# Performance work log

Measured on AMD Instinct MI355X. Metric: run time of the kernel, lower is better.

The kernel has to match this reference:

```python
import jax, jax.numpy as jnp
import numpy as np

# Static problem sizes
B, C, T, H, W = 2, 256, 16, 64, 64
N = 128                      # number of ROIs
OT, OH, OW = 2, 7, 7         # output_size (t, h, w)
SS, TS = 1.0, 1.0            # spatial_scale, temporal_scale
T_EXT_MAX, S_EXT_MAX = 16, 32  # max ROI extents (by construction of rois)
# adaptive_max_pool bin length is bounded by ceil(L/O)+1
KT = (T_EXT_MAX + OT - 1) // OT + 1   # 9
KS = (S_EXT_MAX + OH - 1) // OH + 1   # 6


def setup_inputs() -> dict:
    key = jax.random.key(0)
    features = jax.random.normal(key, (B, C, T, H, W), dtype=jnp.float32)
    rng = np.random.default_rng(0)
    bidx = rng.integers(0, B, N)
    te = rng.integers(4, T_EXT_MAX + 1, N)
    t1 = rng.integers(0, T - te + 1)
    t2 = t1 + te - 1
    he = rng.integers(8, S_EXT_MAX + 1, N)
    y1 = rng.integers(0, H - he + 1)
    y2 = y1 + he - 1
    we = rng.integers(8, S_EXT_MAX + 1, N)
    x1 = rng.integers(0, W - we + 1)
    x2 = x1 + we - 1
    # layout: (batch_idx, t1, x1, y1, t2, x2, y2)
    rois = np.stack([bidx, t1, x1, y1, t2, x2, y2], axis=1).astype(np.float32)
    return {"features": features, "rois": jnp.asarray(rois)}


def _bin_idx(start, length, O, K):
    """Adaptive-pool bin indices for one dim. Returns abs indices [O,K] and validity mask."""
    o = jnp.arange(O)
    s = (o * length) // O                      # floor(o*L/O)
    e = ((o + 1) * length + O - 1) // O        # ceil((o+1)*L/O)
    idx = s[:, None] + jnp.arange(K)[None, :]  # [O, K]
    valid = idx < e[:, None]
    return start + jnp.minimum(idx, length - 1), valid


def _pool_one(roi, features):
    b = roi[0].astype(jnp.int32)
    # source scales coords cols [1,2,3,4] by spatial_scale and [0,5] by temporal_scale
    scale = jnp.array([TS, SS, SS, SS, SS, TS], dtype=roi.dtype)
    c = jnp.floor(roi[1:7] * scale).astype(jnp.int32)
    t1, x1, y1, t2, x2, y2 = c[0], c[1], c[2], c[3], c[4], c[5]
    feat = features[b]  # [C, T, H, W]
    neg = -jnp.inf
    # W dimension
    wi, wv = _bin_idx(x1, x2 - x1 + 1, OW, KS)
    x = feat[:, :, :, wi]                                    # [C,T,H,OW,KS]
    x = jnp.where(wv, x, neg).max(axis=-1)                   # [C,T,H,OW]
    # H dimension
    hi, hv = _bin_idx(y1, y2 - y1 + 1, OH, KS)
    x = jnp.take(x, hi.reshape(-1), axis=2).reshape(C, T, OH, KS, OW)
    x = jnp.where(hv[None, None, :, :, None], x, neg).max(axis=3)  # [C,T,OH,OW]
    # T dimension
    ti, tv = _bin_idx(t1, t2 - t1 + 1, OT, KT)
    x = jnp.take(x, ti.reshape(-1), axis=1).reshape(C, OT, KT, OH, OW)
    return jnp.where(tv[None, :, :, None, None], x, neg).max(axis=2)  # [C,OT,OH,OW]


def reference(features, rois):
    # sequential map over ROIs keeps peak memory bounded (each ROI pool is fully vectorized)
    return jax.lax.map(lambda r: _pool_one(r, features), rois)  # [N,C,OT,OH,OW]
```

## Files before the change

### kernel.cpp

```cpp
#include <hip/hip_runtime.h>
#include <hip/hip_fp16.h>
#include <math.h>

#define BB 2
#define CC 256
#define TT 16
#define HH 64
#define WW 64
#define NN 128
#define OT 2
#define OH 7
#define OW 7
#define PP (TT * HH * WW)
#define BIN (OT * OH * OW)
#define CU2 (CC / 2)
#define GRIDP (NN * OH * OW / 4)

typedef _Float16 hf2 __attribute__((ext_vector_type(2)));

__global__ __launch_bounds__(256) void transpose_f16_kernel(
    const float* __restrict__ in, unsigned int* __restrict__ outt )
{
    __shared__ float tile[64][65];
    int pb = blockIdx.x & 1023;
    int cb = (blockIdx.x >> 10) & 3;
    int b  = blockIdx.x >> 12;

    int tx = threadIdx.x & 63;
    int wv = threadIdx.x >> 6;
    const float* src = in + ((size_t)b * CC + cb * 64) * PP + pb * 64;
    #pragma unroll
    for (int r = 0; r < 16; ++r) {
        int c = wv + r * 4;
        tile[tx][c] = src[(size_t)c * PP + tx];
    }
    __syncthreads();

    int cp   = threadIdx.x & 31;
    int prow = threadIdx.x >> 5;
    size_t base = ((size_t)b * PP + (size_t)pb * 64) * CC + cb * 64;
    #pragma unroll
    for (int r = 0; r < 8; ++r) {
        int p = prow + r * 8;
        __half h0 = __float2half(tile[p][2 * cp]);
        __half h1 = __float2half(tile[p][2 * cp + 1]);
        unsigned int u = (unsigned int)__half_as_ushort(h0)
                       | ((unsigned int)__half_as_ushort(h1) << 16);
        outt[(base + (size_t)p * CC) / 2 + cp] = u;
    }
}

template<int NX>
__device__ __forceinline__ void pool_loop(
    const unsigned int* __restrict__ p, int niter, int ny,
    int ystep, int tstep, hf2& m0, hf2& m1, hf2& m2, hf2& m3)
{
    uint4 va[NX], vb[NX], vc[NX];
    int iy = 0;

#define PLOAD(dst)                                          \
    _Pragma("unroll")                                       \
    for (int j = 0; j < NX; ++j)                            \
        dst[j] = *(const uint4*)(p + j * CU2);

#define PADV()                                              \
    do { if (++iy == ny) { iy = 0; p += tstep; } else p += ystep; } while (0)

#define PCONSUME(src)                                       \
    _Pragma("unroll")                                       \
    for (int j = 0; j < NX; ++j) {                          \
        m0 = __builtin_elementwise_max(m0, __builtin_bit_cast(hf2, src[j].x)); \
        m1 = __builtin_elementwise_max(m1, __builtin_bit_cast(hf2, src[j].y)); \
        m2 = __builtin_elementwise_max(m2, __builtin_bit_cast(hf2, src[j].z)); \
        m3 = __builtin_elementwise_max(m3, __builtin_bit_cast(hf2, src[j].w)); \
    }

    PLOAD(va); PADV();
    PLOAD(vb); PADV();
    PLOAD(vc); PADV();

    int M   = (niter - 3) / 3;
    int rem = (niter - 3) % 3;
    for (int s = 0; s < M; ++s) {
        PCONSUME(va); PLOAD(va); PADV();
        PCONSUME(vb); PLOAD(vb); PADV();
        PCONSUME(vc); PLOAD(vc); PADV();
    }
    if (rem == 1) {
        PCONSUME(va); PLOAD(va); PADV();
        PCONSUME(vb); PCONSUME(vc); PCONSUME(va);
    } else if (rem == 2) {
        PCONSUME(va); PLOAD(va); PADV();
        PCONSUME(vb); PLOAD(vb); PADV();
        PCONSUME(vc); PCONSUME(va); PCONSUME(vb);
    } else {
        PCONSUME(va); PCONSUME(vb); PCONSUME(vc);
    }
#undef PLOAD
#undef PADV
#undef PCONSUME
}

__global__ __launch_bounds__(256) void roipool3d_f16_kernel(
    const unsigned int* __restrict__ featt,
    const float* __restrict__ rois,
    float* __restrict__ out)
{
    int wg  = blockIdx.x;
    int swz = (wg & 7) * (GRIDP / 8) + (wg >> 3);
    int q    = swz * 4 + (threadIdx.x >> 6);
    int lane = threadIdx.x & 63;
    int half = lane >> 5;
    int cl   = lane & 31;
    int rem  = q % (OH * OW);
    int n    = q / (OH * OW);
    int oh   = rem / OW;
    int ow   = rem % OW;

    const float* r = rois + n * 7;
    int b  = (int)r[0];
    int t1 = (int)r[1];
    int x1 = (int)r[2];
    int y1 = (int)r[3];
    int t2 = (int)r[4];
    int x2 = (int)r[5];
    int y2 = (int)r[6];
    int lt = t2 - t1 + 1, lh = y2 - y1 + 1, lw = x2 - x1 + 1;

    int nt = (lt + 1) >> 1;
    int t0 = t1 + (half ? (lt >> 1) : 0);
    int hs = (oh * lh) / OH, he = ((oh + 1) * lh + OH - 1) / OH;
    int ws = (ow * lw) / OW, we = ((ow + 1) * lw + OW - 1) / OW;
    int ny = he - hs;
    int nx = we - ws;
    int niter = nt * ny;

    const unsigned int* p = featt
        + (size_t)((size_t)b * PP + (size_t)((t0 * HH + (y1 + hs)) * WW + (x1 + ws))) * CU2
        + cl * 4;

    const int ystep = WW * CU2;
    const int tstep = (HH - (ny - 1)) * WW * CU2;

    hf2 m0; m0[0] = (_Float16)(-65504.0f); m0[1] = m0[0];
    hf2 m1 = m0, m2 = m0, m3 = m0;

    switch (nx) {
        case 2: pool_loop<2>(p, niter, ny, ystep, tstep, m0, m1, m2, m3); break;
        case 3: pool_loop<3>(p, niter, ny, ystep, tstep, m0, m1, m2, m3); break;
        case 4: pool_loop<4>(p, niter, ny, ystep, tstep, m0, m1, m2, m3); break;
        case 5: pool_loop<5>(p, niter, ny, ystep, tstep, m0, m1, m2, m3); break;
        default: pool_loop<6>(p, niter, ny, ystep, tstep, m0, m1, m2, m3); break;
    }

    int c0 = cl * 8;
    int bin = half * (OH * OW) + rem;
    size_t ob = (size_t)(n * CC + c0) * BIN + bin;
    out[ob]           = (float)m0[0];
    out[ob + BIN]     = (float)m0[1];
    out[ob + 2 * BIN] = (float)m1[0];
    out[ob + 3 * BIN] = (float)m1[1];
    out[ob + 4 * BIN] = (float)m2[0];
    out[ob + 5 * BIN] = (float)m2[1];
    out[ob + 6 * BIN] = (float)m3[0];
    out[ob + 7 * BIN] = (float)m3[1];
}

#define NXCD 8
#define C_PER_XCD (CC / NXCD)
#define PLANE (NN * BIN)
#define BLOCKS_PER_C (PLANE / 256)
__global__ __launch_bounds__(256) void roipool3d_fb_kernel(
    const float* __restrict__ feat, const float* __restrict__ rois,
    float* __restrict__ out)
{
    int wg = blockIdx.x, xcd = wg % NXCD, i = wg / NXCD;
    int c = xcd * C_PER_XCD + i / BLOCKS_PER_C;
    int p = (i % BLOCKS_PER_C) * 256 + threadIdx.x;
    int n = p / BIN, rem = p % BIN;
    int ot = rem / (OH * OW), oh = (rem / OW) % OH, ow = rem % OW;
    const float* r = rois + n * 7;
    int b = (int)r[0], t1 = (int)r[1], x1 = (int)r[2], y1 = (int)r[3];
    int t2 = (int)r[4], x2 = (int)r[5], y2 = (int)r[6];
    int lt = t2 - t1 + 1, lh = y2 - y1 + 1, lw = x2 - x1 + 1;
    int ts = (ot * lt) / OT, te = ((ot + 1) * lt + OT - 1) / OT;
    int hs = (oh * lh) / OH, he = ((oh + 1) * lh + OH - 1) / OH;
    int ws = (ow * lw) / OW, we = ((ow + 1) * lw + OW - 1) / OW;
    const float* fbase = feat + ((size_t)b * CC + c) * PP;
    float m = -INFINITY;
    for (int t = t1 + ts; t < t1 + te; ++t)
        for (int y = y1 + hs; y < y1 + he; ++y)
            for (int x = x1 + ws; x < x1 + we; ++x)
                m = fmaxf(m, fbase[t * (HH * WW) + y * WW + x]);
    out[((size_t)n * CC + c) * BIN + rem] = m;
}

extern "C" void kernel_launch(void* const* d_in, const int* in_sizes, int n_in,
                              void* d_out, int out_size, void* d_ws, size_t ws_size,
                              hipStream_t stream) {
    const float* feat = (const float*)d_in[0];
    const float* rois = (const float*)d_in[1];
    float* out = (float*)d_out;

    size_t need = (size_t)BB * CC * PP * sizeof(unsigned short);
    if (ws_size >= need && d_ws) {
        unsigned int* featt = (unsigned int*)d_ws;
        transpose_f16_kernel<<<BB * 4 * 1024, 256, 0, stream>>>(feat, featt);
        roipool3d_f16_kernel<<<GRIDP, 256, 0, stream>>>(featt, rois, out);
    } else {
        roipool3d_fb_kernel<<<NXCD * C_PER_XCD * BLOCKS_PER_C, 256, 0, stream>>>(
            feat, rois, out);
    }
}
```

Baseline: 88.44 us.

## Split temporal range across two waves and tune prefetch depth per width

Each output position is now processed by two waves that each cover half of the temporal range, with partial maxima merged through shared memory after a block barrier. The grid doubles in size and each wave's serial load chain is shorter, which should hide memory latency better. The software prefetch depth is now a template parameter chosen per bin width, so narrower bins keep more loads in flight. The cost is an extra barrier, shared-memory traffic, and more register pressure for the deeper buffers.

```diff
diff --git a/kernel.cpp b/kernel.cpp
--- a/kernel.cpp
+++ b/kernel.cpp
@@ -14,7 +14,8 @@
 #define PP (TT * HH * WW)
 #define BIN (OT * OH * OW)
 #define CU2 (CC / 2)
-#define GRIDP (NN * OH * OW / 4)
+#define NQ (NN * OH * OW)
+#define GRIDP (NQ / 2)
 
 typedef _Float16 hf2 __attribute__((ext_vector_type(2)));
 
@@ -50,55 +51,51 @@
     }
 }
 
-template<int NX>
+template<int NX, int D>
 __device__ __forceinline__ void pool_loop(
     const unsigned int* __restrict__ p, int niter, int ny,
     int ystep, int tstep, hf2& m0, hf2& m1, hf2& m2, hf2& m3)
 {
-    uint4 va[NX], vb[NX], vc[NX];
+    uint4 v[D][NX];
     int iy = 0;
 
-#define PLOAD(dst)                                          \
+#define PLOAD(d)                                            \
     _Pragma("unroll")                                       \
     for (int j = 0; j < NX; ++j)                            \
-        dst[j] = *(const uint4*)(p + j * CU2);
+        v[d][j] = *(const uint4*)(p + j * CU2);
 
 #define PADV()                                              \
     do { if (++iy == ny) { iy = 0; p += tstep; } else p += ystep; } while (0)
 
-#define PCONSUME(src)                                       \
+#define PCONS(d)                                            \
     _Pragma("unroll")                                       \
     for (int j = 0; j < NX; ++j) {                          \
-        m0 = __builtin_elementwise_max(m0, __builtin_bit_cast(hf2, src[j].x)); \
-        m1 = __builtin_elementwise_max(m1, __builtin_bit_cast(hf2, src[j].y)); \
-        m2 = __builtin_elementwise_max(m2, __builtin_bit_cast(hf2, src[j].z)); \
-        m3 = __builtin_elementwise_max(m3, __builtin_bit_cast(hf2, src[j].w)); \
-    }
-
-    PLOAD(va); PADV();
-    PLOAD(vb); PADV();
-    PLOAD(vc); PADV();
-
-    int M   = (niter - 3) / 3;
-    int rem = (niter - 3) % 3;
-    for (int s = 0; s < M; ++s) {
-        PCONSUME(va); PLOAD(va); PADV();
-        PCONSUME(vb); PLOAD(vb); PADV();
-        PCONSUME(vc); PLOAD(vc); PADV();
-    }
-    if (rem == 1) {
-        PCONSUME(va); PLOAD(va); PADV();
-        PCONSUME(vb); PCONSUME(vc); PCONSUME(va);
-    } else if (rem == 2) {
-        PCONSUME(va); PLOAD(va); PADV();
-        PCONSUME(vb); PLOAD(vb); PADV();
-        PCONSUME(vc); PCONSUME(va); PCONSUME(vb);
+        m0 = __builtin_elementwise_max(m0, __builtin_bit_cast(hf2, v[d][j].x)); \
+        m1 = __builtin_elementwise_max(m1, __builtin_bit_cast(hf2, v[d][j].y)); \
+        m2 = __builtin_elementwise_max(m2, __builtin_bit_cast(hf2, v[d][j].z)); \
+        m3 = __builtin_elementwise_max(m3, __builtin_bit_cast(hf2, v[d][j].w)); \
+    }
+
+    if (niter > D) {
+        #pragma unroll
+        for (int d = 0; d < D; ++d) { PLOAD(d); PADV(); }
+        int M = (niter - D) / D;
+        int r = (niter - D) % D;
+        for (int s = 0; s < M; ++s) {
+            #pragma unroll
+            for (int d = 0; d < D; ++d) { PCONS(d); PLOAD(d); PADV(); }
+        }
+        #pragma unroll
+        for (int d = 0; d < D - 1; ++d)
+            if (d < r) { PCONS(d); PLOAD(d); PADV(); }
+        #pragma unroll
+        for (int d = 0; d < D; ++d) PCONS(d);
     } else {
-        PCONSUME(va); PCONSUME(vb); PCONSUME(vc);
+        for (int i = 0; i < niter; ++i) { PLOAD(0); PADV(); PCONS(0); }
     }
 #undef PLOAD
 #undef PADV
-#undef PCONSUME
+#undef PCONS
 }
 
 __global__ __launch_bounds__(256) void roipool3d_f16_kernel(
@@ -106,12 +103,17 @@
     const float* __restrict__ rois,
     float* __restrict__ out)
 {
+    __shared__ unsigned int comb[2][64][4];
+
     int wg  = blockIdx.x;
     int swz = (wg & 7) * (GRIDP / 8) + (wg >> 3);
-    int q    = swz * 4 + (threadIdx.x >> 6);
+    int wave  = threadIdx.x >> 6;
+    int qslot = wave >> 1;
+    int tc    = wave & 1;
     int lane = threadIdx.x & 63;
     int half = lane >> 5;
     int cl   = lane & 31;
+    int q    = swz * 2 + qslot;
     int rem  = q % (OH * OW);
     int n    = q / (OH * OW);
     int oh   = rem / OW;
@@ -127,13 +129,16 @@
     int y2 = (int)r[6];
     int lt = t2 - t1 + 1, lh = y2 - y1 + 1, lw = x2 - x1 + 1;
 
-    int nt = (lt + 1) >> 1;
-    int t0 = t1 + (half ? (lt >> 1) : 0);
+    int nt_full = (lt + 1) >> 1;
+    int ntc0 = (nt_full + 1) >> 1;
+    int nt_c = tc ? (nt_full - ntc0) : ntc0;
+    int t0 = t1 + (half ? (lt >> 1) : 0) + (tc ? ntc0 : 0);
+
     int hs = (oh * lh) / OH, he = ((oh + 1) * lh + OH - 1) / OH;
     int ws = (ow * lw) / OW, we = ((ow + 1) * lw + OW - 1) / OW;
     int ny = he - hs;
     int nx = we - ws;
-    int niter = nt * ny;
+    int niter = nt_c * ny;
 
     const unsigned int* p = featt
         + (size_t)((size_t)b * PP + (size_t)((t0 * HH + (y1 + hs)) * WW + (x1 + ws))) * CU2
@@ -146,24 +151,38 @@
     hf2 m1 = m0, m2 = m0, m3 = m0;
 
     switch (nx) {
-        case 2: pool_loop<2>(p, niter, ny, ystep, tstep, m0, m1, m2, m3); break;
-        case 3: pool_loop<3>(p, niter, ny, ystep, tstep, m0, m1, m2, m3); break;
-        case 4: pool_loop<4>(p, niter, ny, ystep, tstep, m0, m1, m2, m3); break;
-        case 5: pool_loop<5>(p, niter, ny, ystep, tstep, m0, m1, m2, m3); break;
-        default: pool_loop<6>(p, niter, ny, ystep, tstep, m0, m1, m2, m3); break;
-    }
-
-    int c0 = cl * 8;
-    int bin = half * (OH * OW) + rem;
-    size_t ob = (size_t)(n * CC + c0) * BIN + bin;
-    out[ob]           = (float)m0[0];
-    out[ob + BIN]     = (float)m0[1];
-    out[ob + 2 * BIN] = (float)m1[0];
-    out[ob + 3 * BIN] = (float)m1[1];
-    out[ob + 4 * BIN] = (float)m2[0];
-    out[ob + 5 * BIN] = (float)m2[1];
-    out[ob + 6 * BIN] = (float)m3[0];
-    out[ob + 7 * BIN] = (float)m3[1];
+        case 2:  pool_loop<2, 6>(p, niter, ny, ystep, tstep, m0, m1, m2, m3); break;
+        case 3:  pool_loop<3, 4>(p, niter, ny, ystep, tstep, m0, m1, m2, m3); break;
+        case 4:  pool_loop<4, 3>(p, niter, ny, ystep, tstep, m0, m1, m2, m3); break;
+        case 5:  pool_loop<5, 2>(p, niter, ny, ystep, tstep, m0, m1, m2, m3); break;
+        default: pool_loop<6, 2>(p, niter, ny, ystep, tstep, m0, m1, m2, m3); break;
+    }
+
+    if (tc) {
+        comb[qslot][lane][0] = __builtin_bit_cast(unsigned int, m0);
+        comb[qslot][lane][1] = __builtin_bit_cast(unsigned int, m1);
+        comb[qslot][lane][2] = __builtin_bit_cast(unsigned int, m2);
+        comb[qslot][lane][3] = __builtin_bit_cast(unsigned int, m3);
+    }
+    __syncthreads();
+    if (!tc) {
+        m0 = __builtin_elementwise_max(m0, __builtin_bit_cast(hf2, comb[qslot][lane][0]));
+        m1 = __builtin_elementwise_max(m1, __builtin_bit_cast(hf2, comb[qslot][lane][1]));
+        m2 = __builtin_elementwise_max(m2, __builtin_bit_cast(hf2, comb[qslot][lane][2]));
+        m3 = __builtin_elementwise_max(m3, __builtin_bit_cast(hf2, comb[qslot][lane][3]));
+
+        int c0 = cl * 8;
+        int bin = half * (OH * OW) + rem;
+        size_t ob = (size_t)(n * CC + c0) * BIN + bin;
+        out[ob]           = (float)m0[0];
+        out[ob + BIN]     = (float)m0[1];
+        out[ob + 2 * BIN] = (float)m1[0];
+        out[ob + 3 * BIN] = (float)m1[1];
+        out[ob + 4 * BIN] = (float)m2[0];
+        out[ob + 5 * BIN] = (float)m2[1];
+        out[ob + 6 * BIN] = (float)m3[0];
+        out[ob + 7 * BIN] = (float)m3[1];
+    }
 }
 
 #define NXCD 8
```

New measurement: 84.11 us. 1.05x faster.
